# Kernel optimization log

Hardware: AMD Instinct MI355X
Metric: run time of the kernel (lower is better)

The kernel has to match this reference:

```python
import jax, jax.numpy as jnp
import numpy as np

IN_CH, OUT_CH, HEADS = 256, 128, 4
DIM_HEAD = OUT_CH // HEADS  # 32 (module overrides dim_head = out_ch // heads)
R = 16  # reduce_size
EPS = 1e-5


def _conv3d(x, w, groups=1, pad=0):
    return jax.lax.conv_general_dilated(
        x, w, (1, 1, 1), [(pad, pad)] * 3,
        dimension_numbers=('NCDHW', 'OIDHW', 'NCDHW'),
        feature_group_count=groups)


def _dwsep(x, wd, wp):
    # depthwise 3x3x3 (groups=C) then pointwise 1x1x1, both bias-free
    y = _conv3d(x, wd, groups=x.shape[1], pad=1)
    return _conv3d(y, wp)


def _bn(x, g, b):
    # training-mode BatchNorm3d: biased batch stats over (N, D, H, W)
    m = x.mean(axis=(0, 2, 3, 4), keepdims=True)
    v = x.var(axis=(0, 2, 3, 4), keepdims=True)
    return (x - m) * jax.lax.rsqrt(v + EPS) * g.reshape(1, -1, 1, 1, 1) + b.reshape(1, -1, 1, 1, 1)


def _interp1(x, axis, out_len):
    in_len = x.shape[axis]
    if in_len == out_len:
        return x
    pos = jnp.arange(out_len, dtype=x.dtype) * ((in_len - 1) / (out_len - 1))  # align_corners=True
    lo = jnp.clip(jnp.floor(pos).astype(jnp.int32), 0, in_len - 1)
    hi = jnp.clip(lo + 1, 0, in_len - 1)
    w = pos - lo.astype(x.dtype)
    shp = [1] * x.ndim
    shp[axis] = out_len
    w = w.reshape(shp)
    return jnp.take(x, lo, axis=axis) * (1 - w) + jnp.take(x, hi, axis=axis) * w


def _interp3(x, size):
    for ax, s in zip((2, 3, 4), size):
        x = _interp1(x, ax, s)
    return x


def _rel_index(h, w, d):
    c = np.stack(np.meshgrid(np.arange(h), np.arange(w), np.arange(d), indexing='ij')).reshape(3, -1)
    rel = (c[:, :, None] - c[:, None, :]).transpose(1, 2, 0).astype(np.int64)
    rel[:, :, 0] += h - 1
    rel[:, :, 1] += w - 1
    rel[:, :, 0] *= 2 * h - 1
    idx = rel.sum(-1)
    # faithful to torch: negative indices wrap around the table
    return idx % ((2 * h - 1) * (2 * w - 1) * (2 * d - 1))


def _rel_bias(table, h, w, d, H, W, D, heads):
    idx = _rel_index(h, w, d)
    bias = table[idx.reshape(-1)].reshape(h, w, d, h * w, -1)
    bias = jnp.repeat(bias, H // h, axis=0)
    bias = jnp.repeat(bias, W // w, axis=1)
    bias = jnp.repeat(bias, D // d, axis=2)
    return bias.reshape(H * W * D, h * w * d, heads).transpose(2, 0, 1)[None]  # [1,heads,Nq,Nk]


def setup_inputs() -> dict:
    key = jax.random.key(0)
    ks = jax.random.split(key, 12)
    n = lambda k, s: jax.random.normal(k, s, dtype=jnp.float32)
    return {
        'x1': n(ks[0], (1, IN_CH, 8, 8, 8)),
        'x2': n(ks[1], (1, OUT_CH, 16, 16, 16)),
        'w_ch': n(ks[2], (OUT_CH, IN_CH, 1, 1, 1)) * 0.05,
        'b_ch': jnp.zeros((OUT_CH,), jnp.float32),
        'gamma_l': jnp.ones((IN_CH,), jnp.float32), 'beta_l': jnp.zeros((IN_CH,), jnp.float32),
        'gamma_h': jnp.ones((OUT_CH,), jnp.float32), 'beta_h': jnp.zeros((OUT_CH,), jnp.float32),
        'gamma2': jnp.ones((OUT_CH,), jnp.float32), 'beta2': jnp.zeros((OUT_CH,), jnp.float32),
        'kv_dw': n(ks[3], (IN_CH, 1, 3, 3, 3)) * 0.05,
        'kv_pw': n(ks[4], (2 * OUT_CH, IN_CH, 1, 1, 1)) * 0.05,
        'q_dw': n(ks[5], (OUT_CH, 1, 3, 3, 3)) * 0.05,
        'q_pw': n(ks[6], (OUT_CH, OUT_CH, 1, 1, 1)) * 0.05,
        'out_dw': n(ks[7], (OUT_CH, 1, 3, 3, 3)) * 0.05,
        'out_pw': n(ks[8], (OUT_CH, OUT_CH, 1, 1, 1)) * 0.05,
        'w_mlp': n(ks[9], (OUT_CH, OUT_CH, 1, 1, 1)) * 0.05,
        'rel_table': n(ks[10], ((2 * R - 1) ** 3, HEADS)) * 0.02,
    }


def reference(x1, x2, w_ch, b_ch, gamma_l, beta_l, gamma_h, beta_h, gamma2, beta2,
              kv_dw, kv_pw, q_dw, q_pw, out_dw, out_pw, w_mlp, rel_table):
    B, C, H, W, D = x1.shape
    _, _, HH, WH, DH = x2.shape
    residue = _interp3(_conv3d(x1, w_ch) + b_ch.reshape(1, -1, 1, 1, 1), (HH, WH, DH))
    x1n = _bn(x1, gamma_l, beta_l)
    x2n = _bn(x2, gamma_h, beta_h)
    k, v = jnp.split(_dwsep(x1n, kv_dw, kv_pw), 2, axis=1)
    q = _dwsep(x2n, q_dw, q_pw)
    if H != R:
        k = _interp3(k, (R, R, R))
        v = _interp3(v, (R, R, R))

    def heads_split(t, h, w_, d):
        # channel layout is (dim_head, heads)
        t = t.reshape(B, DIM_HEAD, HEADS, h, w_, d)
        return t.transpose(0, 2, 3, 4, 5, 1).reshape(B, HEADS, h * w_ * d, DIM_HEAD)

    qh = heads_split(q, HH, WH, DH)
    kh = heads_split(k, R, R, R)
    vh = heads_split(v, R, R, R)
    attn = jnp.einsum('bhid,bhjd->bhij', qh, kh)
    attn = attn + _rel_bias(rel_table, R, R, R, HH, WH, DH, HEADS)
    attn = jax.nn.softmax(attn * (DIM_HEAD ** -0.5), axis=-1)  # note: bias is scaled too, as in source
    o = jnp.einsum('bhij,bhjd->bhid', attn, vh)
    o = o.reshape(B, HEADS, HH, WH, DH, DIM_HEAD).transpose(0, 5, 1, 2, 3, 4).reshape(B, OUT_CH, HH, WH, DH)
    o = _dwsep(o, out_dw, out_pw)
    o = o + residue
    res2 = o
    o = jax.nn.relu(_bn(o, gamma2, beta2))
    o = _conv3d(o, w_mlp)
    return o + res2
```

## Files before the change

### kernel.cpp

```cpp
#include <hip/hip_runtime.h>
#include <hip/hip_bf16.h>

using f32x4  = __attribute__((ext_vector_type(4))) float;
using bf16x8 = __attribute__((ext_vector_type(8))) short;
using i32x4  = __attribute__((ext_vector_type(4))) int;

static constexpr float SCALE = 0.17677669529663687f;
static constexpr float L2E   = 1.4426950408889634f;
static constexpr float SL    = SCALE * L2E;

__device__ inline int cvtpk(float lo, float hi) {
  int r;
  asm("v_cvt_pk_bf16_f32 %0,%1,%2" : "=v"(r) : "v"(lo), "v"(hi));
  return r;
}

__device__ inline void bred2(float& s, float& ss) {
  #pragma unroll
  for (int off = 32; off; off >>= 1) {
    s  += __shfl_down(s, off, 64);
    ss += __shfl_down(ss, off, 64);
  }
  __shared__ float as_[4], ass_[4];
  int wid = threadIdx.x >> 6;
  if ((threadIdx.x & 63) == 0) { as_[wid] = s; ass_[wid] = ss; }
  __syncthreads();
  s  = as_[0] + as_[1] + as_[2] + as_[3];
  ss = ass_[0] + ass_[1] + ass_[2] + ass_[3];
}

__global__ __launch_bounds__(256) void bnstat_both_kernel(
    const float* __restrict__ x1, const float* __restrict__ x2,
    const float* __restrict__ gl, const float* __restrict__ bl,
    const float* __restrict__ gh, const float* __restrict__ bh,
    float* __restrict__ ab_l, float* __restrict__ ab_h) {
  int b = blockIdx.x;
  const float* src; const float *gamma, *beta; float* ab; int S, C, c;
  if (b < 256) { c = b;       src = x1 + (size_t)c * 512;  S = 512;  C = 256; gamma = gl; beta = bl; ab = ab_l; }
  else         { c = b - 256; src = x2 + (size_t)c * 4096; S = 4096; C = 128; gamma = gh; beta = bh; ab = ab_h; }
  float s = 0.f, ss = 0.f;
  for (int i = threadIdx.x; i < S; i += 256) { float v = src[i]; s += v; ss = fmaf(v, v, ss); }
  bred2(s, ss);
  if (threadIdx.x == 0) {
    float inv = 1.0f / (float)S;
    float m   = s * inv;
    float var = ss * inv - m * m;
    float a   = gamma[c] * rsqrtf(var + 1e-5f);
    ab[c]     = a;
    ab[C + c] = beta[c] - m * a;
  }
}

template<bool AFF>
__device__ inline void dw_body(
    const float* __restrict__ in, const float* __restrict__ w,
    const float* __restrict__ ab, float* __restrict__ out,
    int n, int nn, int n3, int C, int t) {
  int c = t / n3, s = t - c * n3;
  int z = s / nn, r = s - z * nn, y = r / n, x = r - y * n;
  const float* src = in + (size_t)c * n3;
  const float* wc  = w + c * 27;
  float a = 1.f, b = 0.f;
  if (AFF) { a = ab[c]; b = ab[C + c]; }
  float acc = 0.f;
  #pragma unroll
  for (int kd = 0; kd < 3; kd++) {
    int zz = z + kd - 1;
    if (zz < 0 || zz >= n) continue;
    #pragma unroll
    for (int kh = 0; kh < 3; kh++) {
      int yy = y + kh - 1;
      if (yy < 0 || yy >= n) continue;
      #pragma unroll
      for (int kw = 0; kw < 3; kw++) {
        int xx = x + kw - 1;
        if (xx < 0 || xx >= n) continue;
        float v = src[(zz * n + yy) * n + xx];
        if (AFF) v = fmaf(v, a, b);
        acc = fmaf(v, wc[kd * 9 + kh * 3 + kw], acc);
      }
    }
  }
  out[t] = acc;
}

__global__ __launch_bounds__(256) void stageA_kernel(
    const float* __restrict__ x1, const float* __restrict__ x2,
    const float* __restrict__ w_ch, const float* __restrict__ b_ch,
    const float* __restrict__ kv_dw, const float* __restrict__ q_dw,
    const float* __restrict__ ab_l, const float* __restrict__ ab_h,
    float* __restrict__ res8, float* __restrict__ kvdw, float* __restrict__ qdw) {
  int b = blockIdx.x;
  if (b < 128) {
    int oc0 = (b >> 1) * 2;
    int s   = (b & 1) * 256 + threadIdx.x;
    float a0 = 0.f, a1 = 0.f;
    const float* w0 = w_ch + (size_t)oc0 * 256;
    const float* w1 = w0 + 256;
    #pragma unroll 8
    for (int ic = 0; ic < 256; ic++) {
      float x = x1[(size_t)ic * 512 + s];
      a0 = fmaf(w0[ic], x, a0);
      a1 = fmaf(w1[ic], x, a1);
    }
    res8[(size_t)oc0 * 512 + s]       = a0 + b_ch[oc0];
    res8[(size_t)(oc0 + 1) * 512 + s] = a1 + b_ch[oc0 + 1];
  } else if (b < 640) {
    dw_body<true>(x1, kv_dw, ab_l, kvdw, 8, 64, 512, 256, (b - 128) * 256 + threadIdx.x);
  } else {
    dw_body<true>(x2, q_dw, ab_h, qdw, 16, 256, 4096, 128, (b - 640) * 256 + threadIdx.x);
  }
}

__device__ inline void icoef8(int o, int& lo, int& hi, float& w) {
  float p = (float)o * (7.0f / 15.0f);
  int l = (int)floorf(p);
  if (l > 7) l = 7;
  int h = l + 1 > 7 ? 7 : l + 1;
  w  = p - (float)l;
  lo = l; hi = h;
}

__device__ inline float trilin8(const float* __restrict__ p,
                                int z0, int z1, float wz,
                                int y0, int y1, float wy,
                                int x0, int x1, float wx) {
  float c00 = p[(z0*8+y0)*8+x0]*(1.f-wx) + p[(z0*8+y0)*8+x1]*wx;
  float c01 = p[(z0*8+y1)*8+x0]*(1.f-wx) + p[(z0*8+y1)*8+x1]*wx;
  float c10 = p[(z1*8+y0)*8+x0]*(1.f-wx) + p[(z1*8+y0)*8+x1]*wx;
  float c11 = p[(z1*8+y1)*8+x0]*(1.f-wx) + p[(z1*8+y1)*8+x1]*wx;
  float c0 = c00*(1.f-wy) + c01*wy;
  float c1 = c10*(1.f-wy) + c11*wy;
  return c0*(1.f-wz) + c1*wz;
}

__global__ __launch_bounds__(512) void stageB_kernel(
    const float* __restrict__ kvdw, const float* __restrict__ kv_pw,
    const float* __restrict__ qdw, const float* __restrict__ q_pw,
    const float* __restrict__ res8,
    unsigned short* __restrict__ Kb, unsigned short* __restrict__ Vt,
    unsigned short* __restrict__ Qpk, float* __restrict__ r16) {
  __shared__ float sm[2][512];
  int b = blockIdx.x;
  int tid = threadIdx.x;
  if (b < 128) {
    int kc0 = b * 2;
    int s = tid;
    float a0 = 0.f, a1 = 0.f;
    const float* w0 = kv_pw + (size_t)kc0 * 256;
    const float* w1 = w0 + 256;
    #pragma unroll 8
    for (int ic = 0; ic < 256; ic++) {
      float x = kvdw[(size_t)ic * 512 + s];
      a0 = fmaf(w0[ic], x, a0);
      a1 = fmaf(w1[ic], x, a1);
    }
    sm[0][s] = a0; sm[1][s] = a1;
    __syncthreads();
    #pragma unroll
    for (int r = 0; r < 16; r++) {
      int u  = r * 512 + tid;
      int cl = u >> 12, j = u & 4095;
      int z = j >> 8, y = (j >> 4) & 15, x = j & 15;
      int z0,z1,y0,y1,x0,x1; float wz,wy,wx;
      icoef8(z, z0, z1, wz); icoef8(y, y0, y1, wy); icoef8(x, x0, x1, wx);
      float val = trilin8(sm[cl], z0, z1, wz, y0, y1, wy, x0, x1, wx);
      __hip_bfloat16 bv = __float2bfloat16(val);
      unsigned short us = *reinterpret_cast<unsigned short*>(&bv);
      int kc = kc0 + cl;
      int c  = kc & 127;
      int head = c & 3, dh = c >> 2;
      if (kc < 128) {
        int k  = j & 31;
        int jp = (j & ~31) | (((k >> 3) << 2) + (k & 3) + ((k & 4) ? 16 : 0));
        Kb[((size_t)(head << 12) + jp) * 32 + dh] = us;
      } else {
        Vt[((size_t)(head * 32) + dh) * 4096 + j] = us;
      }
    }
  } else if (b < 256) {
    int bb   = b - 128;
    int head = bb >> 5;
    int r2   = bb & 31;
    int dh0  = (r2 >> 3) * 8;
    int i    = (r2 & 7) * 512 + tid;
    float acc[8];
    #pragma unroll
    for (int e = 0; e < 8; e++) acc[e] = 0.f;
    #pragma unroll 4
    for (int ic = 0; ic < 128; ic++) {
      float x = qdw[(size_t)ic * 4096 + i];
      #pragma unroll
      for (int e = 0; e < 8; e++)
        acc[e] = fmaf(q_pw[(size_t)((dh0 + e) * 4 + head) * 128 + ic], x, acc[e]);
    }
    i32x4 pk = { cvtpk(acc[0], acc[1]), cvtpk(acc[2], acc[3]),
                 cvtpk(acc[4], acc[5]), cvtpk(acc[6], acc[7]) };
    *reinterpret_cast<i32x4*>(Qpk + ((size_t)(head << 12) + i) * 32 + dh0) = pk;
  } else {
    int t = (b - 256) * 512 + tid;
    int s = t & 4095, c = t >> 12;
    int z = s >> 8, y = (s >> 4) & 15, x = s & 15;
    int z0,z1,y0,y1,x0,x1; float wz,wy,wx;
    icoef8(z, z0, z1, wz); icoef8(y, y0, y1, wy); icoef8(x, x0, x1, wx);
    r16[t] = trilin8(res8 + c * 512, z0, z1, wz, y0, y1, wy, x0, x1, wx);
  }
}

__global__ __launch_bounds__(512, 4) void attn_mfma_kernel(
    const unsigned short* __restrict__ Qpk, const unsigned short* __restrict__ Kb,
    const unsigned short* __restrict__ Vt, const float* __restrict__ table,
    float* __restrict__ part_o, float* __restrict__ part_m, float* __restrict__ part_l) {
  __shared__ float lut[992];
  __shared__ unsigned short kvs[2][4096];

  int head = blockIdx.x >> 8;
  int rem  = blockIdx.x & 255;
  int qg   = rem >> 3;
  int ksb  = rem & 7;
  int tid  = threadIdx.x;

  for (int u = tid; u < 991; u += 512) {
    int p = (u < 15) ? (u - 15 + 29791) : (u - 15);
    lut[u] = table[p * 4 + head] * SL;
  }

  int w    = tid >> 6;
  int lane = tid & 63;
  int qrow = lane & 15;
  int g    = lane >> 4;
  int i    = qg * 128 + w * 16 + qrow;
  int iz = i >> 8, iy = (i >> 4) & 15, ix = i & 15;
  int lanebase = iz * 31 + iy + ix;
  int gof = ((g >= 2) ? 15 : 0) - 8 * g;

  bf16x8 qf = *(const bf16x8*)(Qpk + ((size_t)(head << 12) + i) * 32 + g * 8);

  const unsigned short* Kh = Kb + (size_t)head * 4096 * 32;
  const unsigned short* Vh = Vt + (size_t)head * 32 * 4096;

  int kt0 = ksb * 16;

  const unsigned short* src;
  size_t sstride;
  if (tid < 256) {
    int key = tid >> 2, s = tid & 3;
    int gp  = s ^ ((key >> 1) & 3);
    src = Kh + (size_t)(kt0 * 32 + key) * 32 + gp * 8;
    sstride = 32 * 32;
  } else {
    int tt = tid - 256;
    int dh = tt >> 2, s = tt & 3;
    int gp = s ^ ((dh >> 1) & 3);
    src = Vh + (size_t)dh * 4096 + kt0 * 32 + gp * 8;
    sstride = 32;
  }
  int t8 = tid * 8;

  int sw    = (qrow >> 1) & 3;
  int k0off = qrow * 32 + ((g ^ sw) * 8);
  int k1off = k0off + 512;
  int v0off = 2048 + k0off;
  int v1off = v0off + 512;

  {
    bf16x8 s0 = *(const bf16x8*)src; src += sstride;
    *(bf16x8*)(&kvs[0][t8]) = s0;
  }
  __syncthreads();

  f32x4 zero = {0.f, 0.f, 0.f, 0.f};
  f32x4 accO0 = zero, accO1 = zero;
  float m2 = -1e30f, lpart = 0.f;
  int cur = 0;

  for (int ktl = 0; ktl < 16; ktl++) {
    int kt = kt0 + ktl;
    bf16x8 stg;
    if (ktl < 15) { stg = *(const bf16x8*)src; src += sstride; }

    bf16x8 kf0 = *(const bf16x8*)(&kvs[cur][k0off]);
    bf16x8 kf1 = *(const bf16x8*)(&kvs[cur][k1off]);
    bf16x8 vf0 = *(const bf16x8*)(&kvs[cur][v0off]);
    bf16x8 vf1 = *(const bf16x8*)(&kvs[cur][v1off]);

    f32x4 accA = __builtin_amdgcn_mfma_f32_16x16x32_bf16(kf0, qf, zero, 0, 0, 0);
    f32x4 accB = __builtin_amdgcn_mfma_f32_16x16x32_bf16(kf1, qf, zero, 0, 0, 0);

    int z0 = kt >> 3, y0 = (kt << 1) & 15;
    int Cc = 495 - 31 * z0 - y0;
    const float* lp = &lut[lanebase + Cc + gof - 7];
    float b0 = lp[0], b1 = lp[1], b2 = lp[2], b3 = lp[3];
    float b4 = lp[4], b5 = lp[5], b6 = lp[6], b7 = lp[7];

    float t0 = fmaf(accA[0], SL, b7);
    float t1 = fmaf(accA[1], SL, b6);
    float t2 = fmaf(accA[2], SL, b5);
    float t3 = fmaf(accA[3], SL, b4);
    float t4 = fmaf(accB[0], SL, b3);
    float t5 = fmaf(accB[1], SL, b2);
    float t6 = fmaf(accB[2], SL, b1);
    float t7 = fmaf(accB[3], SL, b0);

    float cm = fmaxf(fmaxf(fmaxf(t0, t1), fmaxf(t2, t3)),
                     fmaxf(fmaxf(t4, t5), fmaxf(t6, t7)));
    cm = fmaxf(cm, __shfl_xor(cm, 16, 64));
    cm = fmaxf(cm, __shfl_xor(cm, 32, 64));

    if (__any(cm > m2 + 8.f)) {
      float mn   = fmaxf(m2, cm);
      float corr = exp2f(m2 - mn);
      m2 = mn;
      lpart *= corr;
      float c0 = __shfl(corr, g * 4 + 0, 64);
      float c1 = __shfl(corr, g * 4 + 1, 64);
      float c2 = __shfl(corr, g * 4 + 2, 64);
      float c3 = __shfl(corr, g * 4 + 3, 64);
      accO0[0] *= c0; accO0[1] *= c1; accO0[2] *= c2; accO0[3] *= c3;
      accO1[0] *= c0; accO1[1] *= c1; accO1[2] *= c2; accO1[3] *= c3;
    }

    float p0 = exp2f(t0 - m2), p1 = exp2f(t1 - m2);
    float p2 = exp2f(t2 - m2), p3 = exp2f(t3 - m2);
    float p4 = exp2f(t4 - m2), p5 = exp2f(t5 - m2);
    float p6 = exp2f(t6 - m2), p7 = exp2f(t7 - m2);
    lpart += ((p0 + p1) + (p2 + p3)) + ((p4 + p5) + (p6 + p7));

    union { i32x4 i4; bf16x8 s8; } pa;
    pa.i4 = (i32x4){ cvtpk(p0, p1), cvtpk(p2, p3),
                     cvtpk(p4, p5), cvtpk(p6, p7) };

    accO0 = __builtin_amdgcn_mfma_f32_16x16x32_bf16(pa.s8, vf0, accO0, 0, 0, 0);
    accO1 = __builtin_amdgcn_mfma_f32_16x16x32_bf16(pa.s8, vf1, accO1, 0, 0, 0);

    if (ktl < 15) *(bf16x8*)(&kvs[cur ^ 1][t8]) = stg;
    __syncthreads();
    cur ^= 1;
  }

  float lsum = lpart + __shfl_xor(lpart, 16, 64);
  lsum += __shfl_xor(lsum, 32, 64);

  int base = head * 8 + ksb;
  if (g == 0) {
    part_m[base * 4096 + i] = m2;
    part_l[base * 4096 + i] = lsum;
  }
  int i0 = qg * 128 + w * 16 + g * 4;
  *(f32x4*)&part_o[(size_t)(base * 32 + qrow) * 4096 + i0]      = accO0;
  *(f32x4*)&part_o[(size_t)(base * 32 + 16 + qrow) * 4096 + i0] = accO1;
}

__global__ __launch_bounds__(256) void attn_reduce_kernel(
    const float* __restrict__ part_o, const float* __restrict__ part_m,
    const float* __restrict__ part_l, float* __restrict__ o_sp) {
  int t = blockIdx.x * 256 + threadIdx.x;
  int i = t & 4095, head = t >> 12;
  float mk[8], mx = -1e30f;
  #pragma unroll
  for (int ks = 0; ks < 8; ks++) { mk[ks] = part_m[(head*8+ks)*4096 + i]; mx = fmaxf(mx, mk[ks]); }
  float c[8], L = 0.f;
  #pragma unroll
  for (int ks = 0; ks < 8; ks++) {
    c[ks] = exp2f(mk[ks] - mx);
    L = fmaf(c[ks], part_l[(head*8+ks)*4096 + i], L);
  }
  float invL = 1.f / L;
  #pragma unroll
  for (int d = 0; d < 32; d++) {
    float acc = 0.f;
    #pragma unroll
    for (int ks = 0; ks < 8; ks++)
      acc = fmaf(c[ks], part_o[(size_t)((head*8+ks)*32 + d) * 4096 + i], acc);
    o_sp[(size_t)(d * 4 + head) * 4096 + i] = acc * invL;
  }
}

__global__ __launch_bounds__(256) void dw_out_kernel(
    const float* __restrict__ in, const float* __restrict__ w, float* __restrict__ out) {
  dw_body<false>(in, w, nullptr, out, 16, 256, 4096, 128, blockIdx.x * 256 + threadIdx.x);
}

__global__ __launch_bounds__(256) void pw_out_kernel(
    const float* __restrict__ in, const float* __restrict__ w,
    const float* __restrict__ r16, float* __restrict__ res2,
    float* __restrict__ sums) {
  __shared__ float red[4][2][2];
  int oc0 = (blockIdx.x >> 3) * 2;
  int sb  = blockIdx.x & 7;
  int s0  = (sb * 256 + threadIdx.x) * 2;
  float a00 = 0.f, a01 = 0.f, a10 = 0.f, a11 = 0.f;
  const float* w0 = w + (size_t)oc0 * 128;
  const float* w1 = w0 + 128;
  #pragma unroll 8
  for (int ic = 0; ic < 128; ic++) {
    float xa = in[(size_t)ic * 4096 + s0];
    float xb = in[(size_t)ic * 4096 + s0 + 1];
    float wv0 = w0[ic], wv1 = w1[ic];
    a00 = fmaf(wv0, xa, a00); a01 = fmaf(wv0, xb, a01);
    a10 = fmaf(wv1, xa, a10); a11 = fmaf(wv1, xb, a11);
  }
  size_t ob0 = (size_t)oc0 * 4096 + s0;
  size_t ob1 = ob0 + 4096;
  float r00 = a00 + r16[ob0],     r01 = a01 + r16[ob0 + 1];
  float r10 = a10 + r16[ob1],     r11 = a11 + r16[ob1 + 1];
  res2[ob0] = r00; res2[ob0 + 1] = r01;
  res2[ob1] = r10; res2[ob1 + 1] = r11;
  float s_0 = r00 + r01, q_0 = fmaf(r00, r00, r01 * r01);
  float s_1 = r10 + r11, q_1 = fmaf(r10, r10, r11 * r11);
  #pragma unroll
  for (int off = 32; off; off >>= 1) {
    s_0 += __shfl_down(s_0, off, 64); q_0 += __shfl_down(q_0, off, 64);
    s_1 += __shfl_down(s_1, off, 64); q_1 += __shfl_down(q_1, off, 64);
  }
  int wid = threadIdx.x >> 6;
  if ((threadIdx.x & 63) == 0) {
    red[wid][0][0] = s_0; red[wid][0][1] = q_0;
    red[wid][1][0] = s_1; red[wid][1][1] = q_1;
  }
  __syncthreads();
  if (threadIdx.x < 2) {
    int o = threadIdx.x;
    float st = red[0][o][0] + red[1][o][0] + red[2][o][0] + red[3][o][0];
    float qt = red[0][o][1] + red[1][o][1] + red[2][o][1] + red[3][o][1];
    sums[(oc0 + o) * 8 + sb]        = st;
    sums[1024 + (oc0 + o) * 8 + sb] = qt;
  }
}

__global__ __launch_bounds__(256) void pw_mlp_kernel(
    const float* __restrict__ res2, const float* __restrict__ w,
    const float* __restrict__ gamma2, const float* __restrict__ beta2,
    const float* __restrict__ sums, float* __restrict__ out) {
  __shared__ float A[128], Bb[128];
  if (threadIdx.x < 128) {
    int c = threadIdx.x;
    float s = 0.f, q = 0.f;
    #pragma unroll
    for (int sb = 0; sb < 8; sb++) { s += sums[c * 8 + sb]; q += sums[1024 + c * 8 + sb]; }
    float m   = s * (1.0f / 4096.0f);
    float var = q * (1.0f / 4096.0f) - m * m;
    float a   = gamma2[c] * rsqrtf(var + 1e-5f);
    A[c]  = a;
    Bb[c] = beta2[c] - m * a;
  }
  __syncthreads();
  int oc0 = (blockIdx.x >> 3) * 2;
  int sb  = blockIdx.x & 7;
  int s0  = (sb * 256 + threadIdx.x) * 2;
  float a00 = 0.f, a01 = 0.f, a10 = 0.f, a11 = 0.f;
  const float* w0 = w + (size_t)oc0 * 128;
  const float* w1 = w0 + 128;
  #pragma unroll 8
  for (int ic = 0; ic < 128; ic++) {
    float aa = A[ic], bb = Bb[ic];
    float xa = fmaxf(fmaf(res2[(size_t)ic * 4096 + s0], aa, bb), 0.f);
    float xb = fmaxf(fmaf(res2[(size_t)ic * 4096 + s0 + 1], aa, bb), 0.f);
    float wv0 = w0[ic], wv1 = w1[ic];
    a00 = fmaf(wv0, xa, a00); a01 = fmaf(wv0, xb, a01);
    a10 = fmaf(wv1, xa, a10); a11 = fmaf(wv1, xb, a11);
  }
  size_t ob0 = (size_t)oc0 * 4096 + s0;
  size_t ob1 = ob0 + 4096;
  out[ob0]     = a00 + res2[ob0];
  out[ob0 + 1] = a01 + res2[ob0 + 1];
  out[ob1]     = a10 + res2[ob1];
  out[ob1 + 1] = a11 + res2[ob1 + 1];
}

extern "C" void kernel_launch(void* const* d_in, const int* in_sizes, int n_in,
                              void* d_out, int out_size, void* d_ws, size_t ws_size,
                              hipStream_t stream) {
  (void)in_sizes; (void)n_in; (void)out_size; (void)ws_size;
  const float* x1      = (const float*)d_in[0];
  const float* x2      = (const float*)d_in[1];
  const float* w_ch    = (const float*)d_in[2];
  const float* b_ch    = (const float*)d_in[3];
  const float* gamma_l = (const float*)d_in[4];
  const float* beta_l  = (const float*)d_in[5];
  const float* gamma_h = (const float*)d_in[6];
  const float* beta_h  = (const float*)d_in[7];
  const float* gamma2  = (const float*)d_in[8];
  const float* beta2   = (const float*)d_in[9];
  const float* kv_dw   = (const float*)d_in[10];
  const float* kv_pw   = (const float*)d_in[11];
  const float* q_dw    = (const float*)d_in[12];
  const float* q_pw    = (const float*)d_in[13];
  const float* out_dw  = (const float*)d_in[14];
  const float* out_pw  = (const float*)d_in[15];
  const float* w_mlp   = (const float*)d_in[16];
  const float* rtab    = (const float*)d_in[17];

  float* ws = (float*)d_ws;
  float* ab_l = ws + 0;
  float* ab_h = ws + 512;
  float* sums = ws + 768;
  float* res8 = ws + 2816;
  float* kvdw = ws + 68352;
  float* qdw  = ws + 199424;
  unsigned short* Qpk = (unsigned short*)(ws + 723712);
  unsigned short* Kb  = (unsigned short*)(ws + 985856);
  unsigned short* Vt  = (unsigned short*)(ws + 1248000);
  float* r16  = ws + 1510144;
  float* o_sp = ws + 2034432;
  float* odw  = ws + 2558720;
  float* res2 = ws + 3083008;
  float* part_o = ws + 3607296;
  float* part_m = ws + 7801600;
  float* part_l = ws + 7932672;

  bnstat_both_kernel<<<384, 256, 0, stream>>>(x1, x2, gamma_l, beta_l, gamma_h, beta_h,
                                              ab_l, ab_h);
  stageA_kernel<<<2688, 256, 0, stream>>>(x1, x2, w_ch, b_ch, kv_dw, q_dw,
                                          ab_l, ab_h, res8, kvdw, qdw);
  stageB_kernel<<<1280, 512, 0, stream>>>(kvdw, kv_pw, qdw, q_pw, res8,
                                          Kb, Vt, Qpk, r16);
  attn_mfma_kernel<<<1024, 512, 0, stream>>>(Qpk, Kb, Vt, rtab,
                                             part_o, part_m, part_l);
  attn_reduce_kernel<<<64, 256, 0, stream>>>(part_o, part_m, part_l, o_sp);
  dw_out_kernel<<<2048, 256, 0, stream>>>(o_sp, out_dw, odw);
  pw_out_kernel<<<512, 256, 0, stream>>>(odw, out_pw, r16, res2, sums);
  pw_mlp_kernel<<<512, 256, 0, stream>>>(res2, w_mlp, gamma2, beta2, sums, (float*)d_out);
}
```

Measured before the change: 109.1 us.

## Process 64-key tiles per iteration in attention partial kernel

The attention inner loop now stages 64 keys per LDS buffer instead of 32, running eight iterations of four QK MFMAs and four PV MFMAs in place of sixteen iterations of two each. The V tile layout and XOR swizzle change to a 64-wide row to fit the larger tile. The aim is to halve the barriers, max-reductions and rescale checks per key, at the cost of more registers and a larger LDS footprint per buffer.

```diff
diff --git a/kernel.cpp b/kernel.cpp
--- a/kernel.cpp
+++ b/kernel.cpp
@@ -239,29 +239,31 @@
   const unsigned short* Kh = Kb + (size_t)head * 4096 * 32;
   const unsigned short* Vh = Vt + (size_t)head * 32 * 4096;
 
-  int kt0 = ksb * 16;
+  int kt64 = ksb * 8;
 
   const unsigned short* src;
   size_t sstride;
   if (tid < 256) {
     int key = tid >> 2, s = tid & 3;
     int gp  = s ^ ((key >> 1) & 3);
-    src = Kh + (size_t)(kt0 * 32 + key) * 32 + gp * 8;
-    sstride = 32 * 32;
+    src = Kh + (size_t)(kt64 * 64 + key) * 32 + gp * 8;
+    sstride = 64 * 32;
   } else {
     int tt = tid - 256;
-    int dh = tt >> 2, s = tt & 3;
-    int gp = s ^ ((dh >> 1) & 3);
-    src = Vh + (size_t)dh * 4096 + kt0 * 32 + gp * 8;
-    sstride = 32;
+    int dh = tt >> 3, s = tt & 7;
+    int kg = s ^ (dh & 7);
+    src = Vh + (size_t)dh * 4096 + kt64 * 64 + kg * 8;
+    sstride = 64;
   }
   int t8 = tid * 8;
 
   int sw    = (qrow >> 1) & 3;
   int k0off = qrow * 32 + ((g ^ sw) * 8);
-  int k1off = k0off + 512;
-  int v0off = 2048 + k0off;
-  int v1off = v0off + 512;
+  int q7    = qrow & 7;
+  int v00 = 2048 + qrow * 64        + (((0 + g) ^ q7) * 8);
+  int v01 = 2048 + (16 + qrow) * 64 + (((0 + g) ^ q7) * 8);
+  int v10 = 2048 + qrow * 64        + (((4 + g) ^ q7) * 8);
+  int v11 = 2048 + (16 + qrow) * 64 + (((4 + g) ^ q7) * 8);
 
   {
     bf16x8 s0 = *(const bf16x8*)src; src += sstride;
@@ -274,36 +276,53 @@
   float m2 = -1e30f, lpart = 0.f;
   int cur = 0;
 
-  for (int ktl = 0; ktl < 16; ktl++) {
-    int kt = kt0 + ktl;
+  for (int it = 0; it < 8; it++) {
     bf16x8 stg;
-    if (ktl < 15) { stg = *(const bf16x8*)src; src += sstride; }
-
-    bf16x8 kf0 = *(const bf16x8*)(&kvs[cur][k0off]);
-    bf16x8 kf1 = *(const bf16x8*)(&kvs[cur][k1off]);
-    bf16x8 vf0 = *(const bf16x8*)(&kvs[cur][v0off]);
-    bf16x8 vf1 = *(const bf16x8*)(&kvs[cur][v1off]);
-
-    f32x4 accA = __builtin_amdgcn_mfma_f32_16x16x32_bf16(kf0, qf, zero, 0, 0, 0);
-    f32x4 accB = __builtin_amdgcn_mfma_f32_16x16x32_bf16(kf1, qf, zero, 0, 0, 0);
-
-    int z0 = kt >> 3, y0 = (kt << 1) & 15;
-    int Cc = 495 - 31 * z0 - y0;
-    const float* lp = &lut[lanebase + Cc + gof - 7];
-    float b0 = lp[0], b1 = lp[1], b2 = lp[2], b3 = lp[3];
-    float b4 = lp[4], b5 = lp[5], b6 = lp[6], b7 = lp[7];
-
-    float t0 = fmaf(accA[0], SL, b7);
-    float t1 = fmaf(accA[1], SL, b6);
-    float t2 = fmaf(accA[2], SL, b5);
-    float t3 = fmaf(accA[3], SL, b4);
-    float t4 = fmaf(accB[0], SL, b3);
-    float t5 = fmaf(accB[1], SL, b2);
-    float t6 = fmaf(accB[2], SL, b1);
-    float t7 = fmaf(accB[3], SL, b0);
-
-    float cm = fmaxf(fmaxf(fmaxf(t0, t1), fmaxf(t2, t3)),
-                     fmaxf(fmaxf(t4, t5), fmaxf(t6, t7)));
+    if (it < 7) { stg = *(const bf16x8*)src; src += sstride; }
+
+    const unsigned short* kb = &kvs[cur][0];
+    bf16x8 kfA = *(const bf16x8*)(kb + k0off);
+    bf16x8 kfB = *(const bf16x8*)(kb + k0off + 512);
+    bf16x8 kfC = *(const bf16x8*)(kb + k0off + 1024);
+    bf16x8 kfD = *(const bf16x8*)(kb + k0off + 1536);
+    bf16x8 vf00 = *(const bf16x8*)(kb + v00);
+    bf16x8 vf01 = *(const bf16x8*)(kb + v01);
+    bf16x8 vf10 = *(const bf16x8*)(kb + v10);
+    bf16x8 vf11 = *(const bf16x8*)(kb + v11);
+
+    f32x4 accA = __builtin_amdgcn_mfma_f32_16x16x32_bf16(kfA, qf, zero, 0, 0, 0);
+    f32x4 accB = __builtin_amdgcn_mfma_f32_16x16x32_bf16(kfB, qf, zero, 0, 0, 0);
+    f32x4 accC = __builtin_amdgcn_mfma_f32_16x16x32_bf16(kfC, qf, zero, 0, 0, 0);
+    f32x4 accD = __builtin_amdgcn_mfma_f32_16x16x32_bf16(kfD, qf, zero, 0, 0, 0);
+
+    int kt  = ksb * 16 + it * 2;
+    int za  = kt >> 3,        ya = (kt << 1) & 15;
+    int zb  = (kt + 1) >> 3,  yb = ((kt + 1) << 1) & 15;
+    const float* lp0 = &lut[lanebase + (495 - 31 * za - ya) + gof - 7];
+    const float* lp1 = &lut[lanebase + (495 - 31 * zb - yb) + gof - 7];
+
+    float t0 = fmaf(accA[0], SL, lp0[7]);
+    float t1 = fmaf(accA[1], SL, lp0[6]);
+    float t2 = fmaf(accA[2], SL, lp0[5]);
+    float t3 = fmaf(accA[3], SL, lp0[4]);
+    float t4 = fmaf(accB[0], SL, lp0[3]);
+    float t5 = fmaf(accB[1], SL, lp0[2]);
+    float t6 = fmaf(accB[2], SL, lp0[1]);
+    float t7 = fmaf(accB[3], SL, lp0[0]);
+    float t8v  = fmaf(accC[0], SL, lp1[7]);
+    float t9   = fmaf(accC[1], SL, lp1[6]);
+    float t10  = fmaf(accC[2], SL, lp1[5]);
+    float t11  = fmaf(accC[3], SL, lp1[4]);
+    float t12  = fmaf(accD[0], SL, lp1[3]);
+    float t13  = fmaf(accD[1], SL, lp1[2]);
+    float t14  = fmaf(accD[2], SL, lp1[1]);
+    float t15  = fmaf(accD[3], SL, lp1[0]);
+
+    float cm = fmaxf(
+        fmaxf(fmaxf(fmaxf(t0, t1), fmaxf(t2, t3)),
+              fmaxf(fmaxf(t4, t5), fmaxf(t6, t7))),
+        fmaxf(fmaxf(fmaxf(t8v, t9), fmaxf(t10, t11)),
+              fmaxf(fmaxf(t12, t13), fmaxf(t14, t15))));
     cm = fmaxf(cm, __shfl_xor(cm, 16, 64));
     cm = fmaxf(cm, __shfl_xor(cm, 32, 64));
 
@@ -320,20 +339,29 @@
       accO1[0] *= c0; accO1[1] *= c1; accO1[2] *= c2; accO1[3] *= c3;
     }
 
-    float p0 = exp2f(t0 - m2), p1 = exp2f(t1 - m2);
-    float p2 = exp2f(t2 - m2), p3 = exp2f(t3 - m2);
-    float p4 = exp2f(t4 - m2), p5 = exp2f(t5 - m2);
-    float p6 = exp2f(t6 - m2), p7 = exp2f(t7 - m2);
-    lpart += ((p0 + p1) + (p2 + p3)) + ((p4 + p5) + (p6 + p7));
-
-    union { i32x4 i4; bf16x8 s8; } pa;
-    pa.i4 = (i32x4){ cvtpk(p0, p1), cvtpk(p2, p3),
-                     cvtpk(p4, p5), cvtpk(p6, p7) };
-
-    accO0 = __builtin_amdgcn_mfma_f32_16x16x32_bf16(pa.s8, vf0, accO0, 0, 0, 0);
-    accO1 = __builtin_amdgcn_mfma_f32_16x16x32_bf16(pa.s8, vf1, accO1, 0, 0, 0);
-
-    if (ktl < 15) *(bf16x8*)(&kvs[cur ^ 1][t8]) = stg;
+    float p0 = exp2f(t0 - m2),  p1 = exp2f(t1 - m2);
+    float p2 = exp2f(t2 - m2),  p3 = exp2f(t3 - m2);
+    float p4 = exp2f(t4 - m2),  p5 = exp2f(t5 - m2);
+    float p6 = exp2f(t6 - m2),  p7 = exp2f(t7 - m2);
+    float p8 = exp2f(t8v - m2), p9 = exp2f(t9 - m2);
+    float p10 = exp2f(t10 - m2), p11 = exp2f(t11 - m2);
+    float p12 = exp2f(t12 - m2), p13 = exp2f(t13 - m2);
+    float p14 = exp2f(t14 - m2), p15 = exp2f(t15 - m2);
+    lpart += (((p0 + p1) + (p2 + p3)) + ((p4 + p5) + (p6 + p7)))
+           + (((p8 + p9) + (p10 + p11)) + ((p12 + p13) + (p14 + p15)));
+
+    union { i32x4 i4; bf16x8 s8; } pa0, pa1;
+    pa0.i4 = (i32x4){ cvtpk(p0, p1),  cvtpk(p2, p3),
+                      cvtpk(p4, p5),  cvtpk(p6, p7) };
+    pa1.i4 = (i32x4){ cvtpk(p8, p9),  cvtpk(p10, p11),
+                      cvtpk(p12, p13), cvtpk(p14, p15) };
+
+    accO0 = __builtin_amdgcn_mfma_f32_16x16x32_bf16(pa0.s8, vf00, accO0, 0, 0, 0);
+    accO1 = __builtin_amdgcn_mfma_f32_16x16x32_bf16(pa0.s8, vf01, accO1, 0, 0, 0);
+    accO0 = __builtin_amdgcn_mfma_f32_16x16x32_bf16(pa1.s8, vf10, accO0, 0, 0, 0);
+    accO1 = __builtin_amdgcn_mfma_f32_16x16x32_bf16(pa1.s8, vf11, accO1, 0, 0, 0);
+
+    if (it < 7) *(bf16x8*)(&kvs[cur ^ 1][t8]) = stg;
     __syncthreads();
     cur ^= 1;
   }
```

Result: no change. 109.7 us (+0.5%).
